# Kernel optimization log

Hardware: AMD Instinct MI355X
Metric: run time of the kernel (lower is better)

## Reference

```python
import jax, jax.numpy as jnp
import numpy as np

N = 8192       # num nodes == voc_size (action_size)
R = 2          # total_rel
B = 2          # n_basis
D0, D1 = 128, 64  # num_layers = [128, 64]


def setup_inputs() -> dict:
    key = jax.random.key(0)
    k0, k1, k2, k3, k4 = jax.random.split(key, 5)
    adj = jax.random.uniform(k0, (R, N, N), dtype=jnp.float32)  # dense relational adjacency
    basis_weight0 = jax.random.normal(k1, (B, N, D0), dtype=jnp.float32) * (1.0 / np.float32(np.sqrt(N)))
    basis_coeff0 = jax.random.normal(k2, (R, B), dtype=jnp.float32) * 0.5
    basis_weight1 = jax.random.normal(k3, (B, D0, D1), dtype=jnp.float32) * (1.0 / np.float32(np.sqrt(D0)))
    basis_coeff1 = jax.random.normal(k4, (R, B), dtype=jnp.float32) * 0.5
    return {
        "adj": adj,
        "basis_weight0": basis_weight0,
        "basis_coeff0": basis_coeff0,
        "basis_weight1": basis_weight1,
        "basis_coeff1": basis_coeff1,
    }


def reference(adj, basis_weight0, basis_coeff0, basis_weight1, basis_coeff1):
    # Layer 0: inp is None -> tmp = concat(adj_r, axis=1) [N, R*N]; out0 = tmp @ W0_flat.
    # Equivalent fused form: out0 = sum_r adj[r] @ W0[r]  (avoids the [N, R*N] concat).
    W0 = jnp.einsum('rb,bno->rno', basis_coeff0, basis_weight0)   # [R, N, D0]
    out0 = jnp.einsum('rnm,rmo->no', adj, W0)                     # [N, D0]

    # Layer 1: relu then per-relation propagate + relation-wise transform.
    h = jax.nn.relu(out0)                                         # [N, D0]
    W1 = jnp.einsum('rb,bmo->rmo', basis_coeff1, basis_weight1)   # [R, D0, D1]
    msgs = jnp.einsum('rnm,mo->rno', adj, h)                      # [R, N, D0]
    out1 = jnp.einsum('rno,rop->np', msgs, W1)                    # [N, D1]

    # final_rep: concat layer outputs along feature dim, sum over nodes -> [1, D0+D1]
    final_rep = jnp.concatenate([out0, out1], axis=1).sum(axis=0).reshape(1, -1)
    return out1, final_rep
```

## Files before the change

### kernel.cpp

```cpp
#include <hip/hip_runtime.h>

typedef __attribute__((ext_vector_type(4))) float f32x4;
typedef __attribute__((ext_vector_type(8))) short s16x8;

#define ADJ_N 8192

__device__ __forceinline__ unsigned short f2bf(float f) {
  unsigned u = __float_as_uint(f);
  u += 0x7FFFu + ((u >> 16) & 1u);
  return (unsigned short)(u >> 16);
}

__global__ __launch_bounds__(256) void build_B0(
    const float* __restrict__ w0, const float* __restrict__ c0,
    unsigned short* __restrict__ Bsw) {
  const int t = blockIdx.x * 256 + threadIdx.x;
  const int ks = t >> 9;
  const int cg = (t >> 6) & 7;
  const int lane = t & 63;
  const int kb = ks * 32 + ((lane >> 4) << 3);
  const int col = cg * 16 + (lane & 15);
  const int r = kb >> 13;
  const int m = kb & (ADJ_N - 1);
  const float a0 = c0[r * 2 + 0], a1 = c0[r * 2 + 1];
  union { unsigned short v[8]; s16x8 s; } out;
#pragma unroll
  for (int j = 0; j < 8; ++j) {
    const size_t idx = (size_t)(m + j) * 128 + col;
    const float f = a0 * w0[idx] + a1 * w0[(size_t)1048576 + idx];
    out.v[j] = f2bf(f);
  }
  ((s16x8*)Bsw)[t] = out.s;
}

__global__ __launch_bounds__(512) void build_B1(
    const float* __restrict__ p0, const float* __restrict__ w1,
    const float* __restrict__ c1, unsigned short* __restrict__ Bsw1,
    float* __restrict__ frep) {
  __shared__ __align__(16) float hs[32][128];
  __shared__ __align__(16) float w1t[2][64 * 128];
  __shared__ float red[512];
  const int tid = threadIdx.x;
  const int m0 = blockIdx.x * 32;

  float cs = 0.f;
  for (int i = tid; i < 32 * 128; i += 512) {
    const int ml = i >> 7, col = i & 127;
    const size_t base = (size_t)(m0 + ml) * 128 + col;
    float s = 0.f;
#pragma unroll
    for (int sp = 0; sp < 8; ++sp) s += p0[(size_t)sp * 1048576 + base];
    cs += s;
    hs[ml][col] = fmaxf(s, 0.f);
  }
  const float ca[2][2] = {{c1[0], c1[1]}, {c1[2], c1[3]}};
  for (int i = tid; i < 2 * 64 * 128; i += 512) {
    const int rr = i >> 13;
    const int p = (i >> 7) & 63;
    const int o = i & 127;
    const float v = ca[rr][0] * w1[(size_t)o * 64 + p] + ca[rr][1] * w1[8192 + (size_t)o * 64 + p];
    const int ch = (o >> 2) ^ (p & 31);
    w1t[rr][p * 128 + ch * 4 + (o & 3)] = v;
  }
  red[tid] = cs;
  __syncthreads();
  if (tid < 128)
    atomicAdd(&frep[tid], red[tid] + red[tid + 128] + red[tid + 256] + red[tid + 384]);

  for (int idx = tid; idx < 4096; idx += 512) {
    const int p = idx & 63;
    const int ml = (idx >> 6) & 31;
    const int rr = idx >> 11;
    float s = 0.f;
#pragma unroll
    for (int ch = 0; ch < 32; ++ch) {
      const f32x4 hv = *(const f32x4*)&hs[ml][ch * 4];
      const f32x4 wv = *(const f32x4*)((const char*)&w1t[rr][0] +
                                       ((size_t)p * 32 + (ch ^ (p & 31))) * 16);
      s += hv[0] * wv[0] + hv[1] * wv[1] + hv[2] * wv[2] + hv[3] * wv[3];
    }
    const int k = rr * ADJ_N + m0 + ml;
    const int ks = k >> 5, kin = k & 31;
    const int lane = ((kin >> 3) << 4) | (p & 15);
    const int j = kin & 7;
    const int cg = p >> 4;
    Bsw1[(((size_t)ks * 4 + cg) * 64 + lane) * 8 + j] = f2bf(s);
  }
}

template <int BN, bool REV>
__global__ __launch_bounds__(256, 4) void gemm_adj(
    const float* __restrict__ adj, const unsigned short* __restrict__ Bfr,
    float* __restrict__ outp) {
  constexpr int BK = 64;
  constexpr int KRANGE = 2048;
  constexpr int NSTEP = KRANGE / BK;
  constexpr int CGS = BN / 16;
  __shared__ __align__(16) unsigned short Bsb[2][2 * CGS * 512];

  const int bx = blockIdx.x;
  const int mblk = bx >> 3;
  const int split = bx & 7;
  const int n0 = mblk * 64;
  const int k0 = split * KRANGE;
  const int r = k0 >> 13;
  const int m0k = k0 & (ADJ_N - 1);

  const int tid = threadIdx.x;
  const int w = tid >> 6;
  const int lane = tid & 63;
  const int lhi = lane >> 4;
  const int llo = lane & 15;

  const float* __restrict__ adjw = adj + ((size_t)r << 26) +
      (size_t)(n0 + w * 16 + llo) * ADJ_N + m0k + lhi * 8;

  f32x4 acc[CGS];
#pragma unroll
  for (int b = 0; b < CGS; ++b) acc[b] = (f32x4){0.f, 0.f, 0.f, 0.f};

  auto loadA = [&](int step, f32x4 (&dst)[4]) {
#pragma unroll
    for (int kc = 0; kc < 2; ++kc)
#pragma unroll
      for (int h = 0; h < 2; ++h)
        dst[kc * 2 + h] = *(const f32x4*)(adjw + step * BK + kc * 32 + h * 4);
  };

  auto stageB = [&](int buf, int step) {
    const int ksb = (k0 >> 5) + step * 2;
    const unsigned short* g = Bfr + (size_t)ksb * CGS * 512 + w * (CGS / 2) * 512 + lane * 8;
#pragma unroll
    for (int i = 0; i < CGS / 2; ++i) {
      __builtin_amdgcn_global_load_lds(
          (const __attribute__((address_space(1))) void*)(g + i * 512),
          (__attribute__((address_space(3))) void*)((char*)&Bsb[buf][0] +
                                                    (w * (CGS / 2) + i) * 1024),
          16, 0, 0);
    }
  };

  auto compute = [&](int buf, f32x4 (&cur)[4]) {
#pragma unroll
    for (int kc = 0; kc < 2; ++kc) {
      union { unsigned u[4]; s16x8 v; } cv;
      asm("v_cvt_pk_bf16_f32 %0, %1, %2" : "=v"(cv.u[0]) : "v"(cur[kc * 2][0]), "v"(cur[kc * 2][1]));
      asm("v_cvt_pk_bf16_f32 %0, %1, %2" : "=v"(cv.u[1]) : "v"(cur[kc * 2][2]), "v"(cur[kc * 2][3]));
      asm("v_cvt_pk_bf16_f32 %0, %1, %2" : "=v"(cv.u[2]) : "v"(cur[kc * 2 + 1][0]), "v"(cur[kc * 2 + 1][1]));
      asm("v_cvt_pk_bf16_f32 %0, %1, %2" : "=v"(cv.u[3]) : "v"(cur[kc * 2 + 1][2]), "v"(cur[kc * 2 + 1][3]));
#pragma unroll
      for (int fc = 0; fc < CGS; ++fc) {
        const s16x8 b = *(const s16x8*)((const char*)&Bsb[buf][0] +
                                        (((kc * CGS + fc) * 64 + lane) << 4));
        acc[fc] = __builtin_amdgcn_mfma_f32_16x16x32_bf16(cv.v, b, acc[fc], 0, 0, 0);
      }
    }
  };

  f32x4 a0[4], a1[4];
  const int step0 = REV ? NSTEP - 1 : 0;
  loadA(step0, a0);
  stageB(0, step0);
  __syncthreads();

  for (int s2 = 0; s2 < NSTEP; s2 += 2) {
    {
      const int sn = REV ? NSTEP - 2 - s2 : s2 + 1;
      stageB(1, sn);
      loadA(sn, a1);
      compute(0, a0);
      __syncthreads();
    }
    {
      const bool more = (s2 + 2 < NSTEP);
      const int sn = REV ? NSTEP - 3 - s2 : s2 + 2;
      if (more) {
        stageB(0, sn);
        loadA(sn, a0);
      }
      compute(1, a1);
      __syncthreads();
    }
  }

  float* po = outp + ((size_t)split * ADJ_N + (size_t)n0) * BN;
#pragma unroll
  for (int fc = 0; fc < CGS; ++fc)
#pragma unroll
    for (int q = 0; q < 4; ++q)
      po[(size_t)(w * 16 + lhi * 4 + q) * BN + fc * 16 + llo] = acc[fc][q];
}

__global__ __launch_bounds__(256) void reduce_out1(
    const float* __restrict__ p1, float* __restrict__ out1,
    float* __restrict__ frep) {
  __shared__ float red[256];
  const int t = threadIdx.x;
  const int col = t & 63, r0 = t >> 6;
  float cs = 0.f;
  for (int k = 0; k < 8; ++k) {
    const size_t row = (size_t)blockIdx.x * 32 + r0 * 8 + k;
    const size_t idx = row * 64 + col;
    float s = 0.f;
#pragma unroll
    for (int sp = 0; sp < 8; ++sp) s += p1[(size_t)sp * 524288 + idx];
    out1[idx] = s;
    cs += s;
  }
  red[t] = cs;
  __syncthreads();
  if (t < 64)
    atomicAdd(&frep[128 + t], red[t] + red[t + 64] + red[t + 128] + red[t + 192]);
}

extern "C" void kernel_launch(void* const* d_in, const int* in_sizes, int n_in,
                              void* d_out, int out_size, void* d_ws, size_t ws_size,
                              hipStream_t stream) {
  const float* adj = (const float*)d_in[0];
  const float* bw0 = (const float*)d_in[1];
  const float* bc0 = (const float*)d_in[2];
  const float* bw1 = (const float*)d_in[3];
  const float* bc1 = (const float*)d_in[4];
  float* out = (float*)d_out;
  float* frep = out + (size_t)8192 * 64;

  char* ws = (char*)d_ws;
  float* p0 = (float*)ws;
  float* p1 = (float*)(ws + (32u << 20));
  unsigned short* B0 = (unsigned short*)(ws + (48u << 20));
  unsigned short* B1 = (unsigned short*)(ws + (52u << 20));

  hipMemsetAsync(frep, 0, 192 * sizeof(float), stream);

  build_B0<<<1024, 256, 0, stream>>>(bw0, bc0, B0);
  gemm_adj<128, false><<<1024, 256, 0, stream>>>(adj, B0, p0);
  build_B1<<<256, 512, 0, stream>>>(p0, bw1, bc1, B1, frep);
  gemm_adj<64, true><<<1024, 256, 0, stream>>>(adj, B1, p1);
  reduce_out1<<<256, 256, 0, stream>>>(p1, out, frep);
}
```

Measured before the change: 266.9 us.

## Cache bf16 adjacency from first GEMM and reuse it in second GEMM

The first adjacency GEMM now writes the bf16-converted adjacency tile to a workspace buffer while it computes. The second GEMM reads this bf16 copy instead of re-reading and re-converting the fp32 adjacency, which halves its A-operand traffic. Loads and stores of partial sums and the adjacency also switch to nontemporal hints. The cost is an extra 256MB write during the first GEMM. The REV traversal order that was probably meant to reuse L2/MALL between the two GEMMs is dropped.

```diff
diff --git a/kernel.cpp b/kernel.cpp
--- a/kernel.cpp
+++ b/kernel.cpp
@@ -49,7 +49,8 @@
     const size_t base = (size_t)(m0 + ml) * 128 + col;
     float s = 0.f;
 #pragma unroll
-    for (int sp = 0; sp < 8; ++sp) s += p0[(size_t)sp * 1048576 + base];
+    for (int sp = 0; sp < 8; ++sp)
+      s += __builtin_nontemporal_load(&p0[(size_t)sp * 1048576 + base]);
     cs += s;
     hs[ml][col] = fmaxf(s, 0.f);
   }
@@ -88,14 +89,10 @@
   }
 }
 
-template <int BN, bool REV>
-__global__ __launch_bounds__(256, 4) void gemm_adj(
+__global__ __launch_bounds__(256, 4) void gemm1_adj(
     const float* __restrict__ adj, const unsigned short* __restrict__ Bfr,
-    float* __restrict__ outp) {
-  constexpr int BK = 64;
-  constexpr int KRANGE = 2048;
-  constexpr int NSTEP = KRANGE / BK;
-  constexpr int CGS = BN / 16;
+    float* __restrict__ outp, unsigned short* __restrict__ adjB) {
+  constexpr int BN = 128, CGS = 8, BK = 64, KRANGE = 2048, NSTEP = 32;
   __shared__ __align__(16) unsigned short Bsb[2][2 * CGS * 512];
 
   const int bx = blockIdx.x;
@@ -109,11 +106,13 @@
   const int tid = threadIdx.x;
   const int w = tid >> 6;
   const int lane = tid & 63;
-  const int lhi = lane >> 4;
-  const int llo = lane & 15;
-
-  const float* __restrict__ adjw = adj + ((size_t)r << 26) +
-      (size_t)(n0 + w * 16 + llo) * ADJ_N + m0k + lhi * 8;
+  const int lhi = lane >> 4, llo = lane & 15;
+  const int rowa = n0 + w * 16 + llo;
+
+  const float* __restrict__ adjw =
+      adj + ((size_t)r << 26) + (size_t)rowa * ADJ_N + m0k + lhi * 8;
+  unsigned short* __restrict__ adjBw =
+      adjB + ((size_t)r << 26) + (size_t)rowa * ADJ_N + m0k + lhi * 8;
 
   f32x4 acc[CGS];
 #pragma unroll
@@ -124,7 +123,8 @@
     for (int kc = 0; kc < 2; ++kc)
 #pragma unroll
       for (int h = 0; h < 2; ++h)
-        dst[kc * 2 + h] = *(const f32x4*)(adjw + step * BK + kc * 32 + h * 4);
+        dst[kc * 2 + h] = __builtin_nontemporal_load(
+            (const f32x4*)(adjw + step * BK + kc * 32 + h * 4));
   };
 
   auto stageB = [&](int buf, int step) {
@@ -140,7 +140,7 @@
     }
   };
 
-  auto compute = [&](int buf, f32x4 (&cur)[4]) {
+  auto compute = [&](int buf, f32x4 (&cur)[4], int s) {
 #pragma unroll
     for (int kc = 0; kc < 2; ++kc) {
       union { unsigned u[4]; s16x8 v; } cv;
@@ -148,6 +148,7 @@
       asm("v_cvt_pk_bf16_f32 %0, %1, %2" : "=v"(cv.u[1]) : "v"(cur[kc * 2][2]), "v"(cur[kc * 2][3]));
       asm("v_cvt_pk_bf16_f32 %0, %1, %2" : "=v"(cv.u[2]) : "v"(cur[kc * 2 + 1][0]), "v"(cur[kc * 2 + 1][1]));
       asm("v_cvt_pk_bf16_f32 %0, %1, %2" : "=v"(cv.u[3]) : "v"(cur[kc * 2 + 1][2]), "v"(cur[kc * 2 + 1][3]));
+      *(s16x8*)(adjBw + s * BK + kc * 32) = cv.v;
 #pragma unroll
       for (int fc = 0; fc < CGS; ++fc) {
         const s16x8 b = *(const s16x8*)((const char*)&Bsb[buf][0] +
@@ -158,29 +159,104 @@
   };
 
   f32x4 a0[4], a1[4];
-  const int step0 = REV ? NSTEP - 1 : 0;
-  loadA(step0, a0);
-  stageB(0, step0);
+  loadA(0, a0);
+  stageB(0, 0);
   __syncthreads();
 
   for (int s2 = 0; s2 < NSTEP; s2 += 2) {
-    {
-      const int sn = REV ? NSTEP - 2 - s2 : s2 + 1;
-      stageB(1, sn);
-      loadA(sn, a1);
-      compute(0, a0);
-      __syncthreads();
-    }
-    {
-      const bool more = (s2 + 2 < NSTEP);
-      const int sn = REV ? NSTEP - 3 - s2 : s2 + 2;
-      if (more) {
-        stageB(0, sn);
-        loadA(sn, a0);
+    stageB(1, s2 + 1);
+    loadA(s2 + 1, a1);
+    compute(0, a0, s2);
+    __syncthreads();
+    if (s2 + 2 < NSTEP) {
+      stageB(0, s2 + 2);
+      loadA(s2 + 2, a0);
+    }
+    compute(1, a1, s2 + 1);
+    __syncthreads();
+  }
+
+  float* po = outp + ((size_t)split * ADJ_N + (size_t)n0) * BN;
+#pragma unroll
+  for (int fc = 0; fc < CGS; ++fc)
+#pragma unroll
+    for (int q = 0; q < 4; ++q)
+      __builtin_nontemporal_store(
+          acc[fc][q], &po[(size_t)(w * 16 + lhi * 4 + q) * BN + fc * 16 + llo]);
+}
+
+__global__ __launch_bounds__(256, 4) void gemm2_adj(
+    const unsigned short* __restrict__ adjB, const unsigned short* __restrict__ Bfr,
+    float* __restrict__ outp) {
+  constexpr int BN = 64, CGS = 4, BK = 64, KRANGE = 2048, NSTEP = 32;
+  __shared__ __align__(16) unsigned short Bsb[2][2 * CGS * 512];
+
+  const int bx = blockIdx.x;
+  const int mblk = bx >> 3;
+  const int split = bx & 7;
+  const int n0 = mblk * 64;
+  const int k0 = split * KRANGE;
+  const int r = k0 >> 13;
+  const int m0k = k0 & (ADJ_N - 1);
+
+  const int tid = threadIdx.x;
+  const int w = tid >> 6;
+  const int lane = tid & 63;
+  const int lhi = lane >> 4, llo = lane & 15;
+  const int rowa = n0 + w * 16 + llo;
+
+  const unsigned short* __restrict__ adjw =
+      adjB + ((size_t)r << 26) + (size_t)rowa * ADJ_N + m0k + lhi * 8;
+
+  f32x4 acc[CGS];
+#pragma unroll
+  for (int b = 0; b < CGS; ++b) acc[b] = (f32x4){0.f, 0.f, 0.f, 0.f};
+
+  auto loadA = [&](int step, s16x8 (&dst)[2]) {
+    dst[0] = *(const s16x8*)(adjw + step * BK);
+    dst[1] = *(const s16x8*)(adjw + step * BK + 32);
+  };
+
+  auto stageB = [&](int buf, int step) {
+    const int ksb = (k0 >> 5) + step * 2;
+    const unsigned short* g = Bfr + (size_t)ksb * CGS * 512 + w * (CGS / 2) * 512 + lane * 8;
+#pragma unroll
+    for (int i = 0; i < CGS / 2; ++i) {
+      __builtin_amdgcn_global_load_lds(
+          (const __attribute__((address_space(1))) void*)(g + i * 512),
+          (__attribute__((address_space(3))) void*)((char*)&Bsb[buf][0] +
+                                                    (w * (CGS / 2) + i) * 1024),
+          16, 0, 0);
+    }
+  };
+
+  auto compute = [&](int buf, s16x8 (&cur)[2]) {
+#pragma unroll
+    for (int kc = 0; kc < 2; ++kc)
+#pragma unroll
+      for (int fc = 0; fc < CGS; ++fc) {
+        const s16x8 b = *(const s16x8*)((const char*)&Bsb[buf][0] +
+                                        (((kc * CGS + fc) * 64 + lane) << 4));
+        acc[fc] = __builtin_amdgcn_mfma_f32_16x16x32_bf16(cur[kc], b, acc[fc], 0, 0, 0);
       }
-      compute(1, a1);
-      __syncthreads();
-    }
+  };
+
+  s16x8 a0[2], a1[2];
+  loadA(0, a0);
+  stageB(0, 0);
+  __syncthreads();
+
+  for (int s2 = 0; s2 < NSTEP; s2 += 2) {
+    stageB(1, s2 + 1);
+    loadA(s2 + 1, a1);
+    compute(0, a0);
+    __syncthreads();
+    if (s2 + 2 < NSTEP) {
+      stageB(0, s2 + 2);
+      loadA(s2 + 2, a0);
+    }
+    compute(1, a1);
+    __syncthreads();
   }
 
   float* po = outp + ((size_t)split * ADJ_N + (size_t)n0) * BN;
@@ -188,7 +264,8 @@
   for (int fc = 0; fc < CGS; ++fc)
 #pragma unroll
     for (int q = 0; q < 4; ++q)
-      po[(size_t)(w * 16 + lhi * 4 + q) * BN + fc * 16 + llo] = acc[fc][q];
+      __builtin_nontemporal_store(
+          acc[fc][q], &po[(size_t)(w * 16 + lhi * 4 + q) * BN + fc * 16 + llo]);
 }
 
 __global__ __launch_bounds__(256) void reduce_out1(
@@ -203,7 +280,8 @@
     const size_t idx = row * 64 + col;
     float s = 0.f;
 #pragma unroll
-    for (int sp = 0; sp < 8; ++sp) s += p1[(size_t)sp * 524288 + idx];
+    for (int sp = 0; sp < 8; ++sp)
+      s += __builtin_nontemporal_load(&p1[(size_t)sp * 524288 + idx]);
     out1[idx] = s;
     cs += s;
   }
@@ -229,12 +307,13 @@
   float* p1 = (float*)(ws + (32u << 20));
   unsigned short* B0 = (unsigned short*)(ws + (48u << 20));
   unsigned short* B1 = (unsigned short*)(ws + (52u << 20));
+  unsigned short* adjB = (unsigned short*)(ws + (64u << 20));
 
   hipMemsetAsync(frep, 0, 192 * sizeof(float), stream);
 
   build_B0<<<1024, 256, 0, stream>>>(bw0, bc0, B0);
-  gemm_adj<128, false><<<1024, 256, 0, stream>>>(adj, B0, p0);
+  gemm1_adj<<<1024, 256, 0, stream>>>(adj, B0, p0, adjB);
   build_B1<<<256, 512, 0, stream>>>(p0, bw1, bc1, B1, frep);
-  gemm_adj<64, true><<<1024, 256, 0, stream>>>(adj, B1, p1);
+  gemm2_adj<<<1024, 256, 0, stream>>>(adjB, B1, p1);
   reduce_out1<<<256, 256, 0, stream>>>(p1, out, frep);
 }
```

Result: slower. 313.2 us (+17.3%).
